# Performance work log

Measured on AMD Instinct MI355X. Metric: run time of the kernel, lower is better.

## Reference

```python
import jax, jax.numpy as jnp
import numpy as np

NEG_SLOPE = 0.2  # PyG GATConv default leaky_relu slope


def _gat_layer(x, src, dst, W, a_src, a_dst, b, N, concat):
    # x: [N, F_in]; W: [F_in, H*C]; a_src/a_dst: [H, C]; b: [H*C] or [C]
    H, C = a_src.shape
    h = (x @ W).reshape(N, H, C)                      # [N, H, C]
    al_s = jnp.einsum('nhc,hc->nh', h, a_src)          # [N, H]
    al_d = jnp.einsum('nhc,hc->nh', h, a_dst)          # [N, H]
    e = jax.nn.leaky_relu(al_s[src] + al_d[dst], NEG_SLOPE)  # [E, H]
    # segment softmax over incoming edges of each dst node
    m = jax.ops.segment_max(e, dst, num_segments=N)    # [N, H]
    ex = jnp.exp(e - m[dst])                           # [E, H]
    denom = jax.ops.segment_sum(ex, dst, num_segments=N)
    attn = ex / denom[dst]                             # [E, H]
    msg = (h[src] * attn[:, :, None]).reshape(-1, H * C)  # [E, H*C]
    out = jax.ops.segment_sum(msg, dst, num_segments=N)   # [N, H*C]
    if concat:
        return out + b
    return out.reshape(N, H, C).mean(axis=1) + b


def setup_inputs() -> dict:
    key = jax.random.key(0)
    ks = jax.random.split(key, 20)
    N, E, D, C, H = 20000, 160000, 768, 128, 4
    HC = H * C  # 512
    def glorot(k, shape):
        fan = shape[0] + shape[-1]
        return jax.random.uniform(k, shape, jnp.float32, -1.0, 1.0) * np.sqrt(6.0 / fan)
    inp = {
        'x': jax.random.normal(ks[0], (N, D), jnp.float32),
        'edge_index': jax.random.randint(ks[1], (2, E), 0, N, jnp.int64),
        'W1': glorot(ks[2], (D, HC)),  'as1': glorot(ks[3], (H, C)), 'ad1': glorot(ks[4], (H, C)), 'b1': jnp.zeros((HC,), jnp.float32),
        'W2': glorot(ks[5], (HC, HC)), 'as2': glorot(ks[6], (H, C)), 'ad2': glorot(ks[7], (H, C)), 'b2': jnp.zeros((HC,), jnp.float32),
        'W3': glorot(ks[8], (HC, C)),  'as3': glorot(ks[9], (1, C)), 'ad3': glorot(ks[10], (1, C)), 'b3': jnp.zeros((C,), jnp.float32),
        'Ws1': glorot(ks[11], (C, C // 2)), 'bs1': jnp.zeros((C // 2,), jnp.float32),
        'Ws2': glorot(ks[12], (C // 2, 1)), 'bs2': jnp.zeros((1,), jnp.float32),
    }
    return inp


def reference(x, edge_index, W1, as1, ad1, b1, W2, as2, ad2, b2, W3, as3, ad3, b3, Ws1, bs1, Ws2, bs2):
    N = x.shape[0]
    loops = jnp.arange(N, dtype=edge_index.dtype)
    src = jnp.concatenate([edge_index[0], loops])  # add self-loops (PyG default)
    dst = jnp.concatenate([edge_index[1], loops])
    h = _gat_layer(x, src, dst, W1, as1, ad1, b1, N, concat=True)
    h = jax.nn.relu(h)  # dropout is identity in eval mode
    h = _gat_layer(h, src, dst, W2, as2, ad2, b2, N, concat=True)
    h = jax.nn.relu(h)
    h = _gat_layer(h, src, dst, W3, as3, ad3, b3, N, concat=False)
    # risk scoring head: Linear -> ReLU -> Linear -> Sigmoid
    s = jax.nn.relu(h @ Ws1 + bs1)
    return jax.nn.sigmoid(s @ Ws2 + bs2)  # [N, 1]
```

## Files before the change

### kernel.cpp

```cpp
#include <hip/hip_runtime.h>
#include <hip/hip_bf16.h>
#include <math.h>

#define NEG_SLOPE 0.2f

typedef __attribute__((ext_vector_type(8))) __bf16 bf16x8;
typedef __attribute__((ext_vector_type(4))) float f32x4;

__device__ inline float lrelu(float v) { return v > 0.f ? v : NEG_SLOPE * v; }

__device__ inline unsigned short f2bf(float f) {
    __hip_bfloat16 h = __float2bfloat16(f);
    return *reinterpret_cast<unsigned short*>(&h);
}
__device__ inline float bf_lo(unsigned u) { return __uint_as_float(u << 16); }
__device__ inline float bf_hi(unsigned u) { return __uint_as_float(u & 0xffff0000u); }

__device__ inline void transpose_one(const float* __restrict__ in,
                                     unsigned short* __restrict__ out,
                                     int K, int N, int idx) {
    if (idx >= K * N) return;
    int n = idx / K, k = idx % K;
    out[(size_t)n * K + k] = f2bf(in[(size_t)k * N + n]);
}

__global__ __launch_bounds__(256) void preproc_kernel(
    const float* __restrict__ W1, unsigned short* __restrict__ W1t,
    const float* __restrict__ W2, unsigned short* __restrict__ W2t,
    const float* __restrict__ W3, unsigned short* __restrict__ W3t,
    const float* __restrict__ Ws1, unsigned short* __restrict__ Ws1t,
    const int* __restrict__ ei, int E, int N, int* __restrict__ deg,
    int c1, int c2, int c3, int c4,
    int D, int HC, int C) {
    int b = blockIdx.x;
    int t = threadIdx.x;
    if (b < c1) { transpose_one(W1, W1t, D, HC, b * 256 + t); return; }
    b -= c1;
    if (b < c2) { transpose_one(W2, W2t, HC, HC, b * 256 + t); return; }
    b -= c2;
    if (b < c3) { transpose_one(W3, W3t, HC, C, b * 256 + t); return; }
    b -= c3;
    if (b < c4) { transpose_one(Ws1, Ws1t, 128, 64, b * 256 + t); return; }
    b -= c4;
    {
        int e = b * 256 + t;
        if (e < E + N) {
            int dst = (e < E) ? ei[E + e] : (e - E);
            atomicAdd(&deg[dst], 1);
        }
    }
}

__global__ void scan_kernel(const int* __restrict__ deg, int* __restrict__ off, int N) {
    __shared__ int sums[1024];
    int tid = threadIdx.x;
    int chunk = (N + 1023) / 1024;
    int start = tid * chunk;
    int end = start + chunk; if (end > N) end = N;
    int s = 0;
#pragma unroll 4
    for (int i = start; i < end && i < N; i++) s += deg[i];
    sums[tid] = s;
    __syncthreads();
    for (int d = 1; d < 1024; d <<= 1) {
        int v = 0;
        if (tid >= d) v = sums[tid - d];
        __syncthreads();
        if (tid >= d) sums[tid] += v;
        __syncthreads();
    }
    int prefix = (tid == 0) ? 0 : sums[tid - 1];
    int run = prefix;
#pragma unroll 4
    for (int i = start; i < end && i < N; i++) { off[i] = run; run += deg[i]; }
    if (tid == 1023) off[N] = sums[1023];
}

__global__ void scatter_kernel(const int* __restrict__ ei, int E, int N,
                               const int* __restrict__ off, int* __restrict__ cursor,
                               int* __restrict__ csr_src) {
    int e = blockIdx.x * blockDim.x + threadIdx.x;
    if (e >= E + N) return;
    int src, dst;
    if (e < E) { src = ei[e]; dst = ei[E + e]; }
    else       { src = dst = e - E; }
    int pos = off[dst] + atomicAdd(&cursor[dst], 1);
    csr_src[pos] = src;
}

template <int HEADS, bool AFP32>
__global__ __launch_bounds__(256) void gemm256(const void* __restrict__ Araw,
                                               const unsigned short* __restrict__ Bt,
                                               unsigned short* __restrict__ Cc,
                                               int M, int N, int K, int rowTiles,
                                               const float* __restrict__ a_src,
                                               const float* __restrict__ a_dst,
                                               float* __restrict__ alS,
                                               float* __restrict__ alD) {
    __shared__ unsigned short Asl[64 * 64];
    __shared__ unsigned short Bsl[256 * 64];
    const int tid  = threadIdx.x;
    const int lane = tid & 63;
    const int wave = tid >> 6;

    int r, c;
    {
        int b = blockIdx.x;
        int mainRows = rowTiles & ~7;
        int mainBlocks = mainRows * 2;
        if (b < mainBlocks) {
            int xcd = b & 7;
            c = (b >> 3) & 1;
            r = (b >> 4) * 8 + xcd;
        } else {
            int idx = b - mainBlocks;
            r = mainRows + (idx >> 1);
            c = idx & 1;
        }
    }
    const int rowBase = r * 64;
    const int colBase = c * 256;
    const int wm = (wave & 1) * 32;
    const int wn = (wave >> 1) * 128;
    const int q   = lane >> 4;
    const int l16 = lane & 15;

    const int r0 = tid >> 3;
    const int cg = (tid & 7) ^ (r0 & 7);

    f32x4 acc[2][8] = {};

    for (int k0 = 0; k0 < K; k0 += 64) {
        if (AFP32) {
            const float* Af = (const float*)Araw;
#pragma unroll
            for (int it = 0; it < 2; it++) {
                int row = it * 32 + r0;
                int ga = rowBase + row; if (ga >= M) ga = M - 1;
                const float* gp = Af + (size_t)ga * K + k0 + (tid & 7) * 8;
                float4 v0 = *reinterpret_cast<const float4*>(gp);
                float4 v1 = *reinterpret_cast<const float4*>(gp + 4);
                ushort4 o0, o1;
                o0.x = f2bf(v0.x); o0.y = f2bf(v0.y); o0.z = f2bf(v0.z); o0.w = f2bf(v0.w);
                o1.x = f2bf(v1.x); o1.y = f2bf(v1.y); o1.z = f2bf(v1.z); o1.w = f2bf(v1.w);
                int sc = (tid & 7) ^ (row & 7);
                ushort4* dp = reinterpret_cast<ushort4*>(&Asl[row * 64 + sc * 8]);
                dp[0] = o0; dp[1] = o1;
            }
        } else {
            const unsigned short* Ab = (const unsigned short*)Araw;
#pragma unroll
            for (int it = 0; it < 2; it++) {
                int s = it * 256 + tid;
                int rr = it * 32 + r0;
                int ga = rowBase + rr; if (ga >= M) ga = M - 1;
                const unsigned short* gpa = Ab + (size_t)ga * K + k0 + cg * 8;
                __builtin_amdgcn_global_load_lds(
                    (const __attribute__((address_space(1))) void*)gpa,
                    (__attribute__((address_space(3))) void*)&Asl[(size_t)s * 8],
                    16, 0, 0);
            }
        }
#pragma unroll
        for (int it = 0; it < 8; it++) {
            int s = it * 256 + tid;
            int rr = it * 32 + r0;
            const unsigned short* gpb = Bt + (size_t)(colBase + rr) * K + k0 + cg * 8;
            __builtin_amdgcn_global_load_lds(
                (const __attribute__((address_space(1))) void*)gpb,
                (__attribute__((address_space(3))) void*)&Bsl[(size_t)s * 8],
                16, 0, 0);
        }
        __syncthreads();

#pragma unroll
        for (int kh = 0; kh < 2; kh++) {
            bf16x8 af[2], bfv[8];
#pragma unroll
            for (int mi = 0; mi < 2; mi++) {
                int row = wm + mi * 16 + l16;
                int ch = (kh * 4 + q) ^ (row & 7);
                af[mi] = *reinterpret_cast<const bf16x8*>(&Asl[row * 64 + ch * 8]);
            }
#pragma unroll
            for (int ni = 0; ni < 8; ni++) {
                int row = wn + ni * 16 + l16;
                int ch = (kh * 4 + q) ^ (row & 7);
                bfv[ni] = *reinterpret_cast<const bf16x8*>(&Bsl[row * 64 + ch * 8]);
            }
#pragma unroll
            for (int mi = 0; mi < 2; mi++)
#pragma unroll
                for (int ni = 0; ni < 8; ni++)
                    acc[mi][ni] = __builtin_amdgcn_mfma_f32_16x16x32_bf16(af[mi], bfv[ni], acc[mi][ni], 0, 0, 0);
        }
        __syncthreads();
    }

    const int hIdx = (colBase + wn) >> 7;
    const int hl   = wn >> 7;
    const float* aslp = a_src + hIdx * 128;
    const float* adlp = a_dst + hIdx * 128;
    float acoef[8], dcoef[8];
#pragma unroll
    for (int ni = 0; ni < 8; ni++) {
        int cl = ni * 16 + l16;
        acoef[ni] = aslp[cl];
        dcoef[ni] = adlp[cl];
    }

    float2* red = reinterpret_cast<float2*>(Asl);

#pragma unroll
    for (int mi = 0; mi < 2; mi++) {
#pragma unroll
        for (int rr = 0; rr < 4; rr++) {
            int lrow = wm + mi * 16 + q * 4 + rr;
            int grow = rowBase + lrow;
            bool ok = grow < M;
            float vs = 0.f, vd = 0.f;
#pragma unroll
            for (int ni = 0; ni < 8; ni++) {
                float hv = acc[mi][ni][rr];
                vs += hv * acoef[ni];
                vd += hv * dcoef[ni];
                if (ok) {
                    int gcol = colBase + wn + ni * 16 + l16;
                    Cc[(size_t)grow * N + gcol] = f2bf(hv);
                }
            }
#pragma unroll
            for (int d = 1; d < 16; d <<= 1) {
                vs += __shfl_xor(vs, d);
                vd += __shfl_xor(vd, d);
            }
            if (l16 == 0) red[lrow * 2 + hl] = make_float2(vs, vd);
        }
    }
    __syncthreads();
    if (tid < 128) {
        int row = tid & 63, hh = tid >> 6;
        int grow = rowBase + row;
        if (grow < M) {
            float2 v = red[row * 2 + hh];
            alS[(size_t)grow * HEADS + (colBase >> 7) + hh] = v.x;
            alD[(size_t)grow * HEADS + (colBase >> 7) + hh] = v.y;
        }
    }
}

template <int HEADS>
__global__ __launch_bounds__(256) void gemm_bf16_alpha(const unsigned short* __restrict__ A,
                                                       const unsigned short* __restrict__ Bt,
                                                       unsigned short* __restrict__ C,
                                                       int M, int N, int K, int rowTiles,
                                                       const float* __restrict__ a_src,
                                                       const float* __restrict__ a_dst,
                                                       float* __restrict__ alS,
                                                       float* __restrict__ alD) {
    __shared__ unsigned short Asl[64 * 64];
    __shared__ unsigned short Bsl[128 * 64];
    const int tid  = threadIdx.x;
    const int lane = tid & 63;
    const int wave = tid >> 6;

    int r = blockIdx.x, c = 0;
    const int rowBase = r * 64;
    const int colBase = c * 128;
    const int wm = (wave & 1) * 32;
    const int wn = (wave >> 1) * 64;
    const int q   = lane >> 4;
    const int l16 = lane & 15;

    const int r0 = tid >> 3;
    const int cg = (tid & 7) ^ (r0 & 7);

    f32x4 acc[2][4] = {};

    for (int k0 = 0; k0 < K; k0 += 64) {
#pragma unroll
        for (int it = 0; it < 2; it++) {
            int s = it * 256 + tid;
            int rr = it * 32 + r0;
            int ga = rowBase + rr; if (ga >= M) ga = M - 1;
            const unsigned short* gpa = A + (size_t)ga * K + k0 + cg * 8;
            __builtin_amdgcn_global_load_lds(
                (const __attribute__((address_space(1))) void*)gpa,
                (__attribute__((address_space(3))) void*)&Asl[(size_t)s * 8],
                16, 0, 0);
        }
#pragma unroll
        for (int it = 0; it < 4; it++) {
            int s = it * 256 + tid;
            int rr = it * 32 + r0;
            const unsigned short* gpb = Bt + (size_t)(colBase + rr) * K + k0 + cg * 8;
            __builtin_amdgcn_global_load_lds(
                (const __attribute__((address_space(1))) void*)gpb,
                (__attribute__((address_space(3))) void*)&Bsl[(size_t)s * 8],
                16, 0, 0);
        }
        __syncthreads();

#pragma unroll
        for (int kh = 0; kh < 2; kh++) {
            bf16x8 af[2], bfv[4];
#pragma unroll
            for (int mi = 0; mi < 2; mi++) {
                int row = wm + mi * 16 + l16;
                int ch = (kh * 4 + q) ^ (row & 7);
                af[mi] = *reinterpret_cast<const bf16x8*>(&Asl[row * 64 + ch * 8]);
            }
#pragma unroll
            for (int ni = 0; ni < 4; ni++) {
                int row = wn + ni * 16 + l16;
                int ch = (kh * 4 + q) ^ (row & 7);
                bfv[ni] = *reinterpret_cast<const bf16x8*>(&Bsl[row * 64 + ch * 8]);
            }
#pragma unroll
            for (int mi = 0; mi < 2; mi++)
#pragma unroll
                for (int ni = 0; ni < 4; ni++)
                    acc[mi][ni] = __builtin_amdgcn_mfma_f32_16x16x32_bf16(af[mi], bfv[ni], acc[mi][ni], 0, 0, 0);
        }
        __syncthreads();
    }

    const int hIdx = colBase >> 7;
    const float* asl = a_src + hIdx * 128;
    const float* adl = a_dst + hIdx * 128;
    float acoef[4], dcoef[4];
#pragma unroll
    for (int ni = 0; ni < 4; ni++) {
        int cl = wn + ni * 16 + l16;
        acoef[ni] = asl[cl];
        dcoef[ni] = adl[cl];
    }

    float2* red = reinterpret_cast<float2*>(Asl);
    const int half = wn >> 6;

#pragma unroll
    for (int mi = 0; mi < 2; mi++) {
#pragma unroll
        for (int rr = 0; rr < 4; rr++) {
            int lrow = wm + mi * 16 + q * 4 + rr;
            int grow = rowBase + lrow;
            bool ok = grow < M;
            float vs = 0.f, vd = 0.f;
#pragma unroll
            for (int ni = 0; ni < 4; ni++) {
                float hv = acc[mi][ni][rr];
                vs += hv * acoef[ni];
                vd += hv * dcoef[ni];
                if (ok) {
                    int gcol = colBase + wn + ni * 16 + l16;
                    C[(size_t)grow * N + gcol] = f2bf(hv);
                }
            }
#pragma unroll
            for (int d = 1; d < 16; d <<= 1) {
                vs += __shfl_xor(vs, d);
                vd += __shfl_xor(vd, d);
            }
            if (l16 == 0) red[lrow * 2 + half] = make_float2(vs, vd);
        }
    }
    __syncthreads();
    if (tid < 64) {
        int grow = rowBase + tid;
        if (grow < M) {
            float2 a = red[tid * 2 + 0];
            float2 b = red[tid * 2 + 1];
            alS[(size_t)grow * HEADS + hIdx] = a.x + b.x;
            alD[(size_t)grow * HEADS + hIdx] = a.y + b.y;
        }
    }
}

template <int H, int C, int MODE>
__global__ __launch_bounds__(256) void gat_aggregate(const unsigned short* __restrict__ hb,
                                                     const float* __restrict__ alS,
                                                     const float* __restrict__ alD,
                                                     const int* __restrict__ off,
                                                     const int* __restrict__ csr_src,
                                                     const float* __restrict__ bias,
                                                     unsigned short* __restrict__ outbuf,
                                                     int N) {
    constexpr int HC = H * C;
    constexpr int PER = HC / 64;
    __shared__ int   sIdx[4][16];
    __shared__ float sW[4][64];

    int n = (blockIdx.x * blockDim.x + threadIdx.x) >> 6;
    int lane = threadIdx.x & 63;
    int wave = threadIdx.x >> 6;
    if (n >= N) return;
    int beg = off[n], end = off[n + 1];

    const int grp  = lane >> 4;
    const int slot = lane & 15;
    const int myh  = (H == 4) ? grp : 0;
    const float adh = alD[n * H + myh];
    const unsigned short* hbl = hb + (size_t)lane * PER;
    const float* sWrow = &sW[wave][grp * 16];

    float m = -1e30f, dn = 0.f;
    float acc0 = 0.f, acc1 = 0.f, acc2 = 0.f, acc3 = 0.f,
          acc4 = 0.f, acc5 = 0.f, acc6 = 0.f, acc7 = 0.f;

    for (int base = beg; base < end; base += 16) {
        int cnt = end - base; if (cnt > 16) cnt = 16;
        bool act = slot < cnt;
        int s_l = csr_src[act ? (base + slot) : base];
        float v = act ? lrelu(alS[s_l * H + myh] + adh) : -1e30f;

        float mc = v;
#pragma unroll
        for (int d = 1; d < 16; d <<= 1) mc = fmaxf(mc, __shfl_xor(mc, d));
        float pl = __expf(v - mc);
        float dc = pl;
#pragma unroll
        for (int d = 1; d < 16; d <<= 1) dc += __shfl_xor(dc, d);
        float nm = fmaxf(m, mc);
        float so = __expf(m - nm);
        float sc = __expf(mc - nm);
        dn = dn * so + dc * sc;
        m = nm;
        float wl = pl * sc;

        if (lane < 16) sIdx[wave][lane] = s_l;
        sW[wave][lane] = wl;

        acc0 *= so; acc1 *= so;
        if (PER == 8) {
            acc2 *= so; acc3 *= so; acc4 *= so; acc5 *= so;
            acc6 *= so; acc7 *= so;
        }

        int cntR = (cnt + 3) & ~3;

        if (PER == 8) {
            int4   sI = *reinterpret_cast<const int4*>(&sIdx[wave][0]);
            float4 wv = *reinterpret_cast<const float4*>(&sWrow[0]);
            uint4 gA0 = *reinterpret_cast<const uint4*>(hbl + (size_t)sI.x * HC);
            uint4 gA1 = *reinterpret_cast<const uint4*>(hbl + (size_t)sI.y * HC);
            uint4 gA2 = *reinterpret_cast<const uint4*>(hbl + (size_t)sI.z * HC);
            uint4 gA3 = *reinterpret_cast<const uint4*>(hbl + (size_t)sI.w * HC);
            for (int i = 0; i < cntR; i += 4) {
                int4 sI2 = {}; float4 wv2 = {};
                uint4 gB0 = {}, gB1 = {}, gB2 = {}, gB3 = {};
                if (i + 4 < cntR) {
                    sI2 = *reinterpret_cast<const int4*>(&sIdx[wave][i + 4]);
                    wv2 = *reinterpret_cast<const float4*>(&sWrow[i + 4]);
                    gB0 = *reinterpret_cast<const uint4*>(hbl + (size_t)sI2.x * HC);
                    gB1 = *reinterpret_cast<const uint4*>(hbl + (size_t)sI2.y * HC);
                    gB2 = *reinterpret_cast<const uint4*>(hbl + (size_t)sI2.z * HC);
                    gB3 = *reinterpret_cast<const uint4*>(hbl + (size_t)sI2.w * HC);
                }
#define CONSUME(G, W)                                                   \
                { uint4 rc = G; float w = W;                            \
                  acc0 += bf_lo(rc.x) * w; acc1 += bf_hi(rc.x) * w;     \
                  acc2 += bf_lo(rc.y) * w; acc3 += bf_hi(rc.y) * w;     \
                  acc4 += bf_lo(rc.z) * w; acc5 += bf_hi(rc.z) * w;     \
                  acc6 += bf_lo(rc.w) * w; acc7 += bf_hi(rc.w) * w; }
                CONSUME(gA0, wv.x); CONSUME(gA1, wv.y);
                CONSUME(gA2, wv.z); CONSUME(gA3, wv.w);
#undef CONSUME
                sI = sI2; wv = wv2;
                gA0 = gB0; gA1 = gB1; gA2 = gB2; gA3 = gB3;
            }
        } else {
            int4   sI = *reinterpret_cast<const int4*>(&sIdx[wave][0]);
            float4 wv = *reinterpret_cast<const float4*>(&sWrow[0]);
            unsigned gA0 = *reinterpret_cast<const unsigned*>(hbl + (size_t)sI.x * HC);
            unsigned gA1 = *reinterpret_cast<const unsigned*>(hbl + (size_t)sI.y * HC);
            unsigned gA2 = *reinterpret_cast<const unsigned*>(hbl + (size_t)sI.z * HC);
            unsigned gA3 = *reinterpret_cast<const unsigned*>(hbl + (size_t)sI.w * HC);
            for (int i = 0; i < cntR; i += 4) {
                int4 sI2 = {}; float4 wv2 = {};
                unsigned gB0 = 0, gB1 = 0, gB2 = 0, gB3 = 0;
                if (i + 4 < cntR) {
                    sI2 = *reinterpret_cast<const int4*>(&sIdx[wave][i + 4]);
                    wv2 = *reinterpret_cast<const float4*>(&sWrow[i + 4]);
                    gB0 = *reinterpret_cast<const unsigned*>(hbl + (size_t)sI2.x * HC);
                    gB1 = *reinterpret_cast<const unsigned*>(hbl + (size_t)sI2.y * HC);
                    gB2 = *reinterpret_cast<const unsigned*>(hbl + (size_t)sI2.z * HC);
                    gB3 = *reinterpret_cast<const unsigned*>(hbl + (size_t)sI2.w * HC);
                }
                acc0 += bf_lo(gA0) * wv.x; acc1 += bf_hi(gA0) * wv.x;
                acc0 += bf_lo(gA1) * wv.y; acc1 += bf_hi(gA1) * wv.y;
                acc0 += bf_lo(gA2) * wv.z; acc1 += bf_hi(gA2) * wv.z;
                acc0 += bf_lo(gA3) * wv.w; acc1 += bf_hi(gA3) * wv.w;
                sI = sI2; wv = wv2;
                gA0 = gB0; gA1 = gB1; gA2 = gB2; gA3 = gB3;
            }
        }
    }

    float invd = 1.f / dn;
    unsigned short* op = outbuf + (size_t)n * HC + lane * PER;
    const float* bp = bias + lane * PER;
    if (PER == 8) {
        float o0 = acc0 * invd + bp[0], o1 = acc1 * invd + bp[1];
        float o2 = acc2 * invd + bp[2], o3 = acc3 * invd + bp[3];
        float o4 = acc4 * invd + bp[4], o5 = acc5 * invd + bp[5];
        float o6 = acc6 * invd + bp[6], o7 = acc7 * invd + bp[7];
        if (MODE == 0) {
            o0 = fmaxf(o0, 0.f); o1 = fmaxf(o1, 0.f); o2 = fmaxf(o2, 0.f); o3 = fmaxf(o3, 0.f);
            o4 = fmaxf(o4, 0.f); o5 = fmaxf(o5, 0.f); o6 = fmaxf(o6, 0.f); o7 = fmaxf(o7, 0.f);
        }
        op[0] = f2bf(o0); op[1] = f2bf(o1); op[2] = f2bf(o2); op[3] = f2bf(o3);
        op[4] = f2bf(o4); op[5] = f2bf(o5); op[6] = f2bf(o6); op[7] = f2bf(o7);
    } else {
        float o0 = acc0 * invd + bp[0], o1 = acc1 * invd + bp[1];
        if (MODE == 0) { o0 = fmaxf(o0, 0.f); o1 = fmaxf(o1, 0.f); }
        op[0] = f2bf(o0); op[1] = f2bf(o1);
    }
}

__global__ __launch_bounds__(256) void head_mfma(const unsigned short* __restrict__ H3,
                                                 const unsigned short* __restrict__ W1t,
                                                 const float* __restrict__ bs1,
                                                 const float* __restrict__ Ws2,
                                                 const float* __restrict__ bs2,
                                                 float* __restrict__ out, int M) {
    __shared__ unsigned short Asl[128 * 128];
    __shared__ unsigned short Bsl[64 * 128];
    const int tid = threadIdx.x, lane = tid & 63, wave = tid >> 6;
    const int q = lane >> 4, l16 = lane & 15;
    const int rowBase = blockIdx.x * 128;
    const int r0 = tid >> 4;
    const int cg = (tid & 15) ^ (r0 & 7);

#pragma unroll
    for (int it = 0; it < 8; it++) {
        int s = it * 256 + tid;
        int r = it * 16 + r0;
        int ga = rowBase + r; if (ga >= M) ga = M - 1;
        const unsigned short* gp = H3 + (size_t)ga * 128 + cg * 8;
        __builtin_amdgcn_global_load_lds(
            (const __attribute__((address_space(1))) void*)gp,
            (__attribute__((address_space(3))) void*)&Asl[(size_t)s * 8], 16, 0, 0);
    }
#pragma unroll
    for (int it = 0; it < 4; it++) {
        int s = it * 256 + tid;
        int r = it * 16 + r0;
        const unsigned short* gp = W1t + (size_t)r * 128 + cg * 8;
        __builtin_amdgcn_global_load_lds(
            (const __attribute__((address_space(1))) void*)gp,
            (__attribute__((address_space(3))) void*)&Bsl[(size_t)s * 8], 16, 0, 0);
    }
    __syncthreads();

    const int wm = wave * 32;
    f32x4 acc[2][4] = {};
#pragma unroll
    for (int kh = 0; kh < 4; kh++) {
        bf16x8 af[2], bfv[4];
#pragma unroll
        for (int mi = 0; mi < 2; mi++) {
            int row = wm + mi * 16 + l16;
            int ch = (kh * 4 + q) ^ (row & 7);
            af[mi] = *reinterpret_cast<const bf16x8*>(&Asl[row * 128 + ch * 8]);
        }
#pragma unroll
        for (int ni = 0; ni < 4; ni++) {
            int row = ni * 16 + l16;
            int ch = (kh * 4 + q) ^ (row & 7);
            bfv[ni] = *reinterpret_cast<const bf16x8*>(&Bsl[row * 128 + ch * 8]);
        }
#pragma unroll
        for (int mi = 0; mi < 2; mi++)
#pragma unroll
            for (int ni = 0; ni < 4; ni++)
                acc[mi][ni] = __builtin_amdgcn_mfma_f32_16x16x32_bf16(af[mi], bfv[ni], acc[mi][ni], 0, 0, 0);
    }
    __syncthreads();

    float b1v[4], w2v[4];
#pragma unroll
    for (int ni = 0; ni < 4; ni++) {
        int cI = ni * 16 + l16;
        b1v[ni] = bs1[cI];
        w2v[ni] = Ws2[cI];
    }
    float* red = reinterpret_cast<float*>(Bsl);
#pragma unroll
    for (int mi = 0; mi < 2; mi++) {
#pragma unroll
        for (int r = 0; r < 4; r++) {
            int lrow = wm + mi * 16 + q * 4 + r;
            float p = 0.f;
#pragma unroll
            for (int ni = 0; ni < 4; ni++)
                p += fmaxf(acc[mi][ni][r] + b1v[ni], 0.f) * w2v[ni];
#pragma unroll
            for (int d = 1; d < 16; d <<= 1) p += __shfl_xor(p, d);
            if (l16 == 0) red[lrow] = p;
        }
    }
    __syncthreads();
    if (tid < 128) {
        int g = rowBase + tid;
        if (g < M) out[g] = 1.f / (1.f + __expf(-(red[tid] + bs2[0])));
    }
}

extern "C" void kernel_launch(void* const* d_in, const int* in_sizes, int n_in,
                              void* d_out, int out_size, void* d_ws, size_t ws_size,
                              hipStream_t stream) {
    const float* x   = (const float*)d_in[0];
    const int*   ei  = (const int*)d_in[1];
    const float* W1  = (const float*)d_in[2];
    const float* as1 = (const float*)d_in[3];
    const float* ad1 = (const float*)d_in[4];
    const float* b1  = (const float*)d_in[5];
    const float* W2  = (const float*)d_in[6];
    const float* as2 = (const float*)d_in[7];
    const float* ad2 = (const float*)d_in[8];
    const float* b2  = (const float*)d_in[9];
    const float* W3  = (const float*)d_in[10];
    const float* as3 = (const float*)d_in[11];
    const float* ad3 = (const float*)d_in[12];
    const float* b3  = (const float*)d_in[13];
    const float* Ws1 = (const float*)d_in[14];
    const float* bs1 = (const float*)d_in[15];
    const float* Ws2 = (const float*)d_in[16];
    const float* bs2 = (const float*)d_in[17];

    const int N = out_size;
    const int E = in_sizes[1] / 2;
    const int D = in_sizes[0] / N;
    const int HC = 512, H = 4, C = 128;
    const int Etot = E + N;

    char* p = (char*)d_ws;
    auto alloc = [&](size_t bytes) -> void* {
        void* q = (void*)p;
        p += (bytes + 255) & ~(size_t)255;
        return q;
    };
    char*  zbeg   = p;
    int*   deg    = (int*)alloc((size_t)N * 4);
    int*   cursor = (int*)alloc((size_t)N * 4);
    char*  zend   = p;
    float* alS1   = (float*)alloc((size_t)N * H * 4);
    float* alD1   = (float*)alloc((size_t)N * H * 4);
    float* alS2   = (float*)alloc((size_t)N * H * 4);
    float* alD2   = (float*)alloc((size_t)N * H * 4);
    float* alS3   = (float*)alloc((size_t)N * 4);
    float* alD3   = (float*)alloc((size_t)N * 4);
    int*   off    = (int*)alloc((size_t)(N + 1) * 4);
    int*   csr    = (int*)alloc((size_t)Etot * 4);
    unsigned short* hbuf = (unsigned short*)alloc((size_t)N * HC * 2);
    unsigned short* h3bf = (unsigned short*)alloc((size_t)N * C * 2);
    unsigned short* obf  = (unsigned short*)alloc((size_t)N * HC * 2);
    unsigned short* W1t  = (unsigned short*)alloc((size_t)D * HC * 2);
    unsigned short* W2t  = (unsigned short*)alloc((size_t)HC * HC * 2);
    unsigned short* W3t  = (unsigned short*)alloc((size_t)HC * C * 2);
    unsigned short* Ws1t = (unsigned short*)alloc((size_t)C * 64 * 2);

    hipMemsetAsync(zbeg, 0, (size_t)(zend - zbeg), stream);

    {
        int c1 = (D * HC + 255) / 256;
        int c2 = (HC * HC + 255) / 256;
        int c3 = (HC * C + 255) / 256;
        int c4 = (128 * 64 + 255) / 256;
        int c5 = (Etot + 255) / 256;
        int total = c1 + c2 + c3 + c4 + c5;
        preproc_kernel<<<total, 256, 0, stream>>>(
            W1, W1t, W2, W2t, W3, W3t, Ws1, Ws1t,
            ei, E, N, deg, c1, c2, c3, c4, D, HC, C);
    }
    scan_kernel<<<1, 1024, 0, stream>>>(deg, off, N);
    scatter_kernel<<<(Etot + 255) / 256, 256, 0, stream>>>(ei, E, N, off, cursor, csr);

    int node_blocks = (N + 3) / 4;
    int rowTiles64 = (N + 63) / 64;
    int headTiles = (N + 127) / 128;

    gemm256<4, true><<<rowTiles64 * 2, 256, 0, stream>>>(
        (const void*)x, W1t, hbuf, N, HC, D, rowTiles64, as1, ad1, alS1, alD1);
    gat_aggregate<4, 128, 0><<<node_blocks, 256, 0, stream>>>(
        hbuf, alS1, alD1, off, csr, b1, obf, N);

    gemm256<4, false><<<rowTiles64 * 2, 256, 0, stream>>>(
        (const void*)obf, W2t, hbuf, N, HC, HC, rowTiles64, as2, ad2, alS2, alD2);
    gat_aggregate<4, 128, 0><<<node_blocks, 256, 0, stream>>>(
        hbuf, alS2, alD2, off, csr, b2, obf, N);

    gemm_bf16_alpha<1><<<rowTiles64, 256, 0, stream>>>(
        obf, W3t, hbuf, N, C, HC, rowTiles64, as3, ad3, alS3, alD3);
    gat_aggregate<1, 128, 2><<<node_blocks, 256, 0, stream>>>(
        hbuf, alS3, alD3, off, csr, b3, h3bf, N);

    head_mfma<<<headTiles, 256, 0, stream>>>(h3bf, Ws1t, bs1, Ws2, bs2, (float*)d_out, N);
}
```

Baseline: 313.7 us.

## Double-buffer LDS tiles in GEMM kernels with manual waitcnt pipelining

Both projection GEMM kernels now keep two LDS buffers and issue the global loads for the next K tile before computing the current one. Explicit s_waitcnt vmcnt and s_barrier replace __syncthreads so that load latency overlaps the MFMA work. This doubles LDS use per block, which may lower occupancy. The loop assumes an even number of K tiles, and hand-counted vmcnt values are fragile if the compiler changes how many loads it emits.

```diff
diff --git a/kernel.cpp b/kernel.cpp
--- a/kernel.cpp
+++ b/kernel.cpp
@@ -88,6 +88,10 @@
     csr_src[pos] = src;
 }
 
+#define BARRIER()   asm volatile("s_barrier" ::: "memory")
+#define WAIT_LGKM0() asm volatile("s_waitcnt lgkmcnt(0)" ::: "memory")
+#define WAIT_VM0()   asm volatile("s_waitcnt vmcnt(0)" ::: "memory")
+
 template <int HEADS, bool AFP32>
 __global__ __launch_bounds__(256) void gemm256(const void* __restrict__ Araw,
                                                const unsigned short* __restrict__ Bt,
@@ -97,8 +101,8 @@
                                                const float* __restrict__ a_dst,
                                                float* __restrict__ alS,
                                                float* __restrict__ alD) {
-    __shared__ unsigned short Asl[64 * 64];
-    __shared__ unsigned short Bsl[256 * 64];
+    __shared__ unsigned short Asl[2][64 * 64];
+    __shared__ unsigned short Bsl[2][256 * 64];
     const int tid  = threadIdx.x;
     const int lane = tid & 63;
     const int wave = tid >> 6;
@@ -128,51 +132,65 @@
     const int r0 = tid >> 3;
     const int cg = (tid & 7) ^ (r0 & 7);
 
+    const int nk = K >> 6;
+
     f32x4 acc[2][8] = {};
 
-    for (int k0 = 0; k0 < K; k0 += 64) {
-        if (AFP32) {
-            const float* Af = (const float*)Araw;
-#pragma unroll
-            for (int it = 0; it < 2; it++) {
-                int row = it * 32 + r0;
-                int ga = rowBase + row; if (ga >= M) ga = M - 1;
-                const float* gp = Af + (size_t)ga * K + k0 + (tid & 7) * 8;
-                float4 v0 = *reinterpret_cast<const float4*>(gp);
-                float4 v1 = *reinterpret_cast<const float4*>(gp + 4);
-                ushort4 o0, o1;
-                o0.x = f2bf(v0.x); o0.y = f2bf(v0.y); o0.z = f2bf(v0.z); o0.w = f2bf(v0.w);
-                o1.x = f2bf(v1.x); o1.y = f2bf(v1.y); o1.z = f2bf(v1.z); o1.w = f2bf(v1.w);
-                int sc = (tid & 7) ^ (row & 7);
-                ushort4* dp = reinterpret_cast<ushort4*>(&Asl[row * 64 + sc * 8]);
-                dp[0] = o0; dp[1] = o1;
-            }
-        } else {
-            const unsigned short* Ab = (const unsigned short*)Araw;
-#pragma unroll
-            for (int it = 0; it < 2; it++) {
-                int s = it * 256 + tid;
-                int rr = it * 32 + r0;
-                int ga = rowBase + rr; if (ga >= M) ga = M - 1;
-                const unsigned short* gpa = Ab + (size_t)ga * K + k0 + cg * 8;
-                __builtin_amdgcn_global_load_lds(
-                    (const __attribute__((address_space(1))) void*)gpa,
-                    (__attribute__((address_space(3))) void*)&Asl[(size_t)s * 8],
-                    16, 0, 0);
-            }
-        }
+    struct ARegs { float4 v[4]; };
+    ARegs RA, RB;
+
+    auto issueB = [&](int kt, int buf) {
 #pragma unroll
         for (int it = 0; it < 8; it++) {
             int s = it * 256 + tid;
             int rr = it * 32 + r0;
-            const unsigned short* gpb = Bt + (size_t)(colBase + rr) * K + k0 + cg * 8;
+            const unsigned short* gpb = Bt + (size_t)(colBase + rr) * K + kt * 64 + cg * 8;
             __builtin_amdgcn_global_load_lds(
                 (const __attribute__((address_space(1))) void*)gpb,
-                (__attribute__((address_space(3))) void*)&Bsl[(size_t)s * 8],
+                (__attribute__((address_space(3))) void*)&Bsl[buf][(size_t)s * 8],
                 16, 0, 0);
         }
-        __syncthreads();
-
+    };
+    auto issueA_lds = [&](int kt, int buf) {
+        const unsigned short* Ab = (const unsigned short*)Araw;
+#pragma unroll
+        for (int it = 0; it < 2; it++) {
+            int s = it * 256 + tid;
+            int rr = it * 32 + r0;
+            int ga = rowBase + rr; if (ga >= M) ga = M - 1;
+            const unsigned short* gpa = Ab + (size_t)ga * K + kt * 64 + cg * 8;
+            __builtin_amdgcn_global_load_lds(
+                (const __attribute__((address_space(1))) void*)gpa,
+                (__attribute__((address_space(3))) void*)&Asl[buf][(size_t)s * 8],
+                16, 0, 0);
+        }
+    };
+    auto loadA = [&](int kt, ARegs& R) {
+        const float* Af = (const float*)Araw;
+#pragma unroll
+        for (int it = 0; it < 2; it++) {
+            int row = it * 32 + r0;
+            int ga = rowBase + row; if (ga >= M) ga = M - 1;
+            const float* gp = Af + (size_t)ga * K + kt * 64 + (tid & 7) * 8;
+            R.v[it * 2 + 0] = *reinterpret_cast<const float4*>(gp);
+            R.v[it * 2 + 1] = *reinterpret_cast<const float4*>(gp + 4);
+        }
+    };
+    auto writeA = [&](ARegs& R, int buf) {
+#pragma unroll
+        for (int it = 0; it < 2; it++) {
+            int row = it * 32 + r0;
+            float4 v0 = R.v[it * 2 + 0];
+            float4 v1 = R.v[it * 2 + 1];
+            ushort4 o0, o1;
+            o0.x = f2bf(v0.x); o0.y = f2bf(v0.y); o0.z = f2bf(v0.z); o0.w = f2bf(v0.w);
+            o1.x = f2bf(v1.x); o1.y = f2bf(v1.y); o1.z = f2bf(v1.z); o1.w = f2bf(v1.w);
+            int sc = (tid & 7) ^ (row & 7);
+            ushort4* dp = reinterpret_cast<ushort4*>(&Asl[buf][row * 64 + sc * 8]);
+            dp[0] = o0; dp[1] = o1;
+        }
+    };
+    auto compute = [&](int buf) {
 #pragma unroll
         for (int kh = 0; kh < 2; kh++) {
             bf16x8 af[2], bfv[8];
@@ -180,13 +198,13 @@
             for (int mi = 0; mi < 2; mi++) {
                 int row = wm + mi * 16 + l16;
                 int ch = (kh * 4 + q) ^ (row & 7);
-                af[mi] = *reinterpret_cast<const bf16x8*>(&Asl[row * 64 + ch * 8]);
+                af[mi] = *reinterpret_cast<const bf16x8*>(&Asl[buf][row * 64 + ch * 8]);
             }
 #pragma unroll
             for (int ni = 0; ni < 8; ni++) {
                 int row = wn + ni * 16 + l16;
                 int ch = (kh * 4 + q) ^ (row & 7);
-                bfv[ni] = *reinterpret_cast<const bf16x8*>(&Bsl[row * 64 + ch * 8]);
+                bfv[ni] = *reinterpret_cast<const bf16x8*>(&Bsl[buf][row * 64 + ch * 8]);
             }
 #pragma unroll
             for (int mi = 0; mi < 2; mi++)
@@ -194,8 +212,37 @@
                 for (int ni = 0; ni < 8; ni++)
                     acc[mi][ni] = __builtin_amdgcn_mfma_f32_16x16x32_bf16(af[mi], bfv[ni], acc[mi][ni], 0, 0, 0);
         }
-        __syncthreads();
-    }
+    };
+#define WAIT_PREV()                                                       \
+    do { if constexpr (AFP32) asm volatile("s_waitcnt vmcnt(12)" ::: "memory"); \
+         else                 asm volatile("s_waitcnt vmcnt(10)" ::: "memory"); } while (0)
+
+    if constexpr (AFP32) loadA(0, RA); else issueA_lds(0, 0);
+    issueB(0, 0);
+
+    for (int kt = 0; kt < nk; kt += 2) {
+        if constexpr (AFP32) loadA(kt + 1, RB); else issueA_lds(kt + 1, 1);
+        issueB(kt + 1, 1);
+        WAIT_PREV();
+        if constexpr (AFP32) { writeA(RA, 0); WAIT_LGKM0(); }
+        BARRIER();
+        compute(0);
+        WAIT_LGKM0();
+        BARRIER();
+        if (kt + 2 < nk) {
+            if constexpr (AFP32) loadA(kt + 2, RA); else issueA_lds(kt + 2, 0);
+            issueB(kt + 2, 0);
+            WAIT_PREV();
+        } else {
+            WAIT_VM0();
+        }
+        if constexpr (AFP32) { writeA(RB, 1); WAIT_LGKM0(); }
+        BARRIER();
+        compute(1);
+        WAIT_LGKM0();
+        BARRIER();
+    }
+#undef WAIT_PREV
 
     const int hIdx = (colBase + wn) >> 7;
     const int hl   = wn >> 7;
@@ -209,7 +256,7 @@
         dcoef[ni] = adlp[cl];
     }
 
-    float2* red = reinterpret_cast<float2*>(Asl);
+    float2* red = reinterpret_cast<float2*>(&Asl[0][0]);
 
 #pragma unroll
     for (int mi = 0; mi < 2; mi++) {
@@ -258,15 +305,15 @@
                                                        const float* __restrict__ a_dst,
                                                        float* __restrict__ alS,
                                                        float* __restrict__ alD) {
-    __shared__ unsigned short Asl[64 * 64];
-    __shared__ unsigned short Bsl[128 * 64];
+    __shared__ unsigned short Asl[2][64 * 64];
+    __shared__ unsigned short Bsl[2][128 * 64];
     const int tid  = threadIdx.x;
     const int lane = tid & 63;
     const int wave = tid >> 6;
 
-    int r = blockIdx.x, c = 0;
+    int r = blockIdx.x;
     const int rowBase = r * 64;
-    const int colBase = c * 128;
+    const int colBase = 0;
     const int wm = (wave & 1) * 32;
     const int wn = (wave >> 1) * 64;
     const int q   = lane >> 4;
@@ -274,33 +321,34 @@
 
     const int r0 = tid >> 3;
     const int cg = (tid & 7) ^ (r0 & 7);
+    const int nk = K >> 6;
 
     f32x4 acc[2][4] = {};
 
-    for (int k0 = 0; k0 < K; k0 += 64) {
+    auto issueTile = [&](int kt, int buf) {
 #pragma unroll
         for (int it = 0; it < 2; it++) {
             int s = it * 256 + tid;
             int rr = it * 32 + r0;
             int ga = rowBase + rr; if (ga >= M) ga = M - 1;
-            const unsigned short* gpa = A + (size_t)ga * K + k0 + cg * 8;
+            const unsigned short* gpa = A + (size_t)ga * K + kt * 64 + cg * 8;
             __builtin_amdgcn_global_load_lds(
                 (const __attribute__((address_space(1))) void*)gpa,
-                (__attribute__((address_space(3))) void*)&Asl[(size_t)s * 8],
+                (__attribute__((address_space(3))) void*)&Asl[buf][(size_t)s * 8],
                 16, 0, 0);
         }
 #pragma unroll
         for (int it = 0; it < 4; it++) {
             int s = it * 256 + tid;
             int rr = it * 32 + r0;
-            const unsigned short* gpb = Bt + (size_t)(colBase + rr) * K + k0 + cg * 8;
+            const unsigned short* gpb = Bt + (size_t)(colBase + rr) * K + kt * 64 + cg * 8;
             __builtin_amdgcn_global_load_lds(
                 (const __attribute__((address_space(1))) void*)gpb,
-                (__attribute__((address_space(3))) void*)&Bsl[(size_t)s * 8],
+                (__attribute__((address_space(3))) void*)&Bsl[buf][(size_t)s * 8],
                 16, 0, 0);
         }
-        __syncthreads();
-
+    };
+    auto compute = [&](int buf) {
 #pragma unroll
         for (int kh = 0; kh < 2; kh++) {
             bf16x8 af[2], bfv[4];
@@ -308,13 +356,13 @@
             for (int mi = 0; mi < 2; mi++) {
                 int row = wm + mi * 16 + l16;
                 int ch = (kh * 4 + q) ^ (row & 7);
-                af[mi] = *reinterpret_cast<const bf16x8*>(&Asl[row * 64 + ch * 8]);
+                af[mi] = *reinterpret_cast<const bf16x8*>(&Asl[buf][row * 64 + ch * 8]);
             }
 #pragma unroll
             for (int ni = 0; ni < 4; ni++) {
                 int row = wn + ni * 16 + l16;
                 int ch = (kh * 4 + q) ^ (row & 7);
-                bfv[ni] = *reinterpret_cast<const bf16x8*>(&Bsl[row * 64 + ch * 8]);
+                bfv[ni] = *reinterpret_cast<const bf16x8*>(&Bsl[buf][row * 64 + ch * 8]);
             }
 #pragma unroll
             for (int mi = 0; mi < 2; mi++)
@@ -322,12 +370,31 @@
                 for (int ni = 0; ni < 4; ni++)
                     acc[mi][ni] = __builtin_amdgcn_mfma_f32_16x16x32_bf16(af[mi], bfv[ni], acc[mi][ni], 0, 0, 0);
         }
-        __syncthreads();
-    }
-
-    const int hIdx = colBase >> 7;
-    const float* asl = a_src + hIdx * 128;
-    const float* adl = a_dst + hIdx * 128;
+    };
+
+    issueTile(0, 0);
+    for (int kt = 0; kt < nk; kt += 2) {
+        issueTile(kt + 1, 1);
+        asm volatile("s_waitcnt vmcnt(6)" ::: "memory");
+        BARRIER();
+        compute(0);
+        WAIT_LGKM0();
+        BARRIER();
+        if (kt + 2 < nk) {
+            issueTile(kt + 2, 0);
+            asm volatile("s_waitcnt vmcnt(6)" ::: "memory");
+        } else {
+            WAIT_VM0();
+        }
+        BARRIER();
+        compute(1);
+        WAIT_LGKM0();
+        BARRIER();
+    }
+
+    const int hIdx = 0;
+    const float* asl = a_src;
+    const float* adl = a_dst;
     float acoef[4], dcoef[4];
 #pragma unroll
     for (int ni = 0; ni < 4; ni++) {
@@ -336,7 +403,7 @@
         dcoef[ni] = adl[cl];
     }
 
-    float2* red = reinterpret_cast<float2*>(Asl);
+    float2* red = reinterpret_cast<float2*>(&Asl[0][0]);
     const int half = wn >> 6;
 
 #pragma unroll
```

Result: slower. 321.8 us (+2.6%).
